# Performance work log

Measured on AMD Instinct MI355X. Metric: run time of the kernel, lower is better.

The kernel has to match this reference:

```python
import jax, jax.numpy as jnp
import numpy as np

NUM_HEADS = 8
EPS = 1e-5


def setup_inputs() -> dict:
    key = jax.random.key(0)
    ks = jax.random.split(key, 7)
    B, C, H, W, D = 1, 256, 16, 16, 16
    return {
        "x": jax.random.normal(ks[0], (B, C, H, W, D), dtype=jnp.float32),
        "w_dw": jax.random.normal(ks[1], (C, 1, 3, 3, 3), dtype=jnp.float32) * 0.05,
        "b_dw": jax.random.normal(ks[2], (C,), dtype=jnp.float32) * 0.05,
        "w_qkv": jax.random.normal(ks[3], (3 * C, C), dtype=jnp.float32) * 0.05,
        "b_qkv": jax.random.normal(ks[4], (3 * C,), dtype=jnp.float32) * 0.05,
        "w_proj": jax.random.normal(ks[5], (C, C), dtype=jnp.float32) * 0.05,
        "b_proj": jax.random.normal(ks[6], (C,), dtype=jnp.float32) * 0.05,
    }


def reference(x, w_dw, b_dw, w_qkv, b_qkv, w_proj, b_proj):
    B, C, H, W, D = x.shape
    nh = NUM_HEADS
    hd = C // nh
    scale = hd ** (-0.5)
    N = H * W * D

    # depthwise 3x3x3 conv (groups=C), SAME padding
    y = jax.lax.conv_general_dilated(
        x, w_dw, window_strides=(1, 1, 1), padding="SAME",
        dimension_numbers=("NCHWD", "OIHWD", "NCHWD"),
        feature_group_count=C,
    ) + b_dw[None, :, None, None, None]

    # InstanceNorm3d (affine=False): normalize over spatial dims per (b, c)
    mu = y.mean(axis=(2, 3, 4), keepdims=True)
    var = y.var(axis=(2, 3, 4), keepdims=True)
    y = (y - mu) * jax.lax.rsqrt(var + EPS)

    # 1x1x1 conv -> 3*C channels
    qkv = jnp.einsum("bchwd,oc->bohwd", y, w_qkv) + b_qkv[None, :, None, None, None]

    # [B, 3, nh, hd, N] -> q, k, v each [B, nh, N, hd]
    qkv = qkv.reshape(B, 3, nh, hd, N)
    q, k, v = jnp.transpose(qkv, (1, 0, 2, 4, 3))

    attn = jax.nn.softmax(jnp.einsum("bhnd,bhmd->bhnm", q, k) * scale, axis=-1)
    out = jnp.einsum("bhnm,bhmd->bhnd", attn, v)  # [B, nh, N, hd]

    # transpose(-1, -2) then reshape to [B, C, H, W, D]
    out = jnp.transpose(out, (0, 1, 3, 2)).reshape(B, C, H, W, D)

    # output 1x1x1 projection
    out = jnp.einsum("bchwd,oc->bohwd", out, w_proj) + b_proj[None, :, None, None, None]
    return out
```

## Files before the change

kernel.cpp:

```cpp
#include <hip/hip_runtime.h>
#include <hip/hip_bf16.h>

#define NSP 4096
#define QSC2 0.25503486f

typedef __attribute__((ext_vector_type(8))) short bf16x8;
typedef __attribute__((ext_vector_type(4))) float f32x4;
typedef __attribute__((ext_vector_type(16))) float f32x16;

__device__ __forceinline__ unsigned short f2bf(float f){
  union{float f;unsigned int u;}c; c.f=f;
  unsigned int r = c.u + 0x7fffu + ((c.u>>16)&1u);
  return (unsigned short)(r>>16);
}
__device__ __forceinline__ unsigned int pk2(float a, float b){
  __hip_bfloat162 p = __float22bfloat162_rn(make_float2(a, b));
  unsigned int r; __builtin_memcpy(&r, &p, 4); return r;
}
__device__ __forceinline__ ushort4 pk4(float a, float b, float c, float d){
  union { ushort4 u4; uint2 u2; } u;
  u.u2.x = pk2(a, b); u.u2.y = pk2(c, d);
  return u.u4;
}

__global__ __launch_bounds__(512) void k_dwconv(
    const float* __restrict__ x,
    const float* __restrict__ wdw,
    const float* __restrict__ bdw,
    unsigned short* __restrict__ ybn)
{
  const int c = blockIdx.x;
  const int tid = threadIdx.x;
  __shared__ float xs[4096];
  __shared__ float wsh[27];
  __shared__ float bsh;
  __shared__ float rs[8], rq[8];

  const float* xc = x + (size_t)c * NSP;
  for (int i = tid; i < 1024; i += 512) *(float4*)&xs[i*4] = ((const float4*)xc)[i];
  if (tid < 27) wsh[tid] = wdw[c*27 + tid];
  if (tid == 31) bsh = bdw[c];
  __syncthreads();

  float yv[8];
  float sum = 0.f, sumsq = 0.f;
  #pragma unroll
  for (int i = 0; i < 8; i++){
    const int n = (i << 9) + tid;
    const int h = n >> 8, w = (n >> 4) & 15, d = n & 15;
    float acc = bsh;
    #pragma unroll
    for (int kh = 0; kh < 3; kh++){
      const int hh = h + kh - 1;
      if ((unsigned)hh >= 16u) continue;
      #pragma unroll
      for (int kw = 0; kw < 3; kw++){
        const int ww = w + kw - 1;
        if ((unsigned)ww >= 16u) continue;
        #pragma unroll
        for (int kd = 0; kd < 3; kd++){
          const int dd = d + kd - 1;
          if ((unsigned)dd >= 16u) continue;
          acc += wsh[kh*9 + kw*3 + kd] * xs[(hh<<8) + (ww<<4) + dd];
        }
      }
    }
    yv[i] = acc; sum += acc; sumsq += acc*acc;
  }
  #pragma unroll
  for (int off = 32; off > 0; off >>= 1){
    sum   += __shfl_down(sum, off, 64);
    sumsq += __shfl_down(sumsq, off, 64);
  }
  const int wid = tid >> 6, lane = tid & 63;
  if (lane == 0){ rs[wid] = sum; rq[wid] = sumsq; }
  __syncthreads();
  float ts = 0.f, tq = 0.f;
  #pragma unroll
  for (int i = 0; i < 8; i++){ ts += rs[i]; tq += rq[i]; }
  const float mean = ts * (1.f/4096.f);
  const float var  = tq * (1.f/4096.f) - mean*mean;
  const float rinv = rsqrtf(var + 1e-5f);
  unsigned short* yo = ybn + (size_t)c * NSP;
  #pragma unroll
  for (int i = 0; i < 8; i++) yo[(i<<9) + tid] = f2bf((yv[i] - mean) * rinv);
}

__global__ __launch_bounds__(256) void k_trans(
    const unsigned short* __restrict__ ybn,
    unsigned short* __restrict__ ynT)
{
  __shared__ unsigned short T[64][72];
  const int tid = threadIdx.x;
  const int n0 = blockIdx.x * 64, c0 = blockIdx.y * 64;
  const int cl = tid >> 4, n4 = (tid & 15) * 4;
  #pragma unroll
  for (int i = 0; i < 4; i++){
    const int c = cl + i*16;
    const ushort4 v = *(const ushort4*)(ybn + (size_t)(c0 + c) * NSP + n0 + n4);
    T[n4+0][c] = v.x; T[n4+1][c] = v.y; T[n4+2][c] = v.z; T[n4+3][c] = v.w;
  }
  __syncthreads();
  const int nl = tid >> 2, s8 = (tid & 3) * 16;
  *(uint4*)(ynT + (size_t)(n0+nl)*256 + c0 + s8)     = *(const uint4*)&T[nl][s8];
  *(uint4*)(ynT + (size_t)(n0+nl)*256 + c0 + s8 + 8) = *(const uint4*)&T[nl][s8 + 8];
}

__global__ __launch_bounds__(256) void k_qkv(
    const float* __restrict__ wqkv,
    const float* __restrict__ bqkv,
    const unsigned short* __restrict__ ynT,
    unsigned short* __restrict__ qb, unsigned short* __restrict__ kb,
    unsigned short* __restrict__ vbt)
{
  __shared__ unsigned short Wb[64][264];
  const int tid = threadIdx.x;
  const int o0 = blockIdx.y * 64;
  const int n0 = blockIdx.x * 128;
  {
    const int row = tid & 63, part = tid >> 6;
    const float* src = wqkv + (size_t)(o0 + row) * 256 + part * 64;
    unsigned short* dst = &Wb[row][part*64];
    #pragma unroll
    for (int j = 0; j < 8; j++){
      const float4 a = ((const float4*)src)[2*j];
      const float4 b = ((const float4*)src)[2*j+1];
      *(ushort4*)&dst[j*8]     = pk4(a.x, a.y, a.z, a.w);
      *(ushort4*)&dst[j*8 + 4] = pk4(b.x, b.y, b.z, b.w);
    }
  }
  __syncthreads();

  const int w = tid >> 6, lane = tid & 63, quad = lane >> 4, cc = lane & 15;
  const int nbase = n0 + w*32;
  const bool isv = (o0 >= 512);
  f32x4 acc[2][4] = {};

  #pragma unroll
  for (int k = 0; k < 8; k++){
    const bf16x8 y0 = *(const bf16x8*)(ynT + (size_t)(nbase + cc)  * 256 + k*32 + quad*8);
    const bf16x8 y1 = *(const bf16x8*)(ynT + (size_t)(nbase+16+cc) * 256 + k*32 + quad*8);
    #pragma unroll
    for (int os = 0; os < 4; os++){
      const bf16x8 wf = *(const bf16x8*)&Wb[os*16 + cc][k*32 + quad*8];
      if (!isv){
        acc[0][os] = __builtin_amdgcn_mfma_f32_16x16x32_bf16(y0, wf, acc[0][os], 0, 0, 0);
        acc[1][os] = __builtin_amdgcn_mfma_f32_16x16x32_bf16(y1, wf, acc[1][os], 0, 0, 0);
      } else {
        acc[0][os] = __builtin_amdgcn_mfma_f32_16x16x32_bf16(wf, y0, acc[0][os], 0, 0, 0);
        acc[1][os] = __builtin_amdgcn_mfma_f32_16x16x32_bf16(wf, y1, acc[1][os], 0, 0, 0);
      }
    }
  }

  if (!isv){
    #pragma unroll
    for (int os = 0; os < 4; os++){
      const int o = o0 + os*16 + cc;
      const int g = o >> 8, hh = (o >> 5) & 7, dd = o & 31;
      const float bias = bqkv[o];
      const float sc = (g == 0) ? QSC2 : 1.f;
      unsigned short* dst = (g == 0) ? qb : kb;
      #pragma unroll
      for (int ns = 0; ns < 2; ns++){
        #pragma unroll
        for (int r = 0; r < 4; r++){
          const int n = nbase + ns*16 + quad*4 + r;
          dst[((size_t)hh * NSP + n) * 32 + dd] = f2bf((acc[ns][os][r] + bias) * sc);
        }
      }
    }
  } else {
    #pragma unroll
    for (int os = 0; os < 4; os++){
      #pragma unroll
      for (int r = 0; r < 4; r++){
        const int orow = o0 - 512 + os*16 + quad*4 + r;
        const float bias = bqkv[512 + orow];
        #pragma unroll
        for (int ns = 0; ns < 2; ns++){
          const int n = nbase + ns*16 + cc;
          vbt[(size_t)orow * NSP + n] = f2bf(acc[ns][os][r] + bias);
        }
      }
    }
  }
}

__global__ __launch_bounds__(128) void k_attn(
    const unsigned short* __restrict__ qb,
    const unsigned short* __restrict__ kb,
    const unsigned short* __restrict__ vbt,
    float* __restrict__ op, float* __restrict__ lp, int ktlen)
{
  const int h = blockIdx.y, q0 = blockIdx.x * 64, z = blockIdx.z;
  const int tid = threadIdx.x;
  const int w = tid >> 6, l = tid & 63;
  const int lq = l & 31, lb = l >> 5;

  __shared__ unsigned short ks [64][40];
  __shared__ unsigned short vsT[32][72];
  __shared__ unsigned short pst[64][72];

  const int qg = q0 + w*32 + lq;
  const bf16x8 qf0 = *(const bf16x8*)(qb + ((size_t)(h*NSP + qg))*32 + lb*8);
  const bf16x8 qf1 = *(const bf16x8*)(qb + ((size_t)(h*NSP + qg))*32 + 16 + lb*8);
  const unsigned short* kbase = kb  + (size_t)h * NSP * 32;
  const unsigned short* vbase = vbt + (size_t)h * 32 * NSP;

  f32x16 oacc = {};
  float lsum = 0.f;

  const int kt0 = z * ktlen;
  const int krow = tid >> 1, kseg = (tid & 1) * 16;
  const int vrow = tid >> 2, vseg = (tid & 3) * 16;
  const int iters = ktlen >> 6;

  for (int it = 0; it < iters; it++){
    const int kt = kt0 + it * 64;
    {
      const uint4* src = (const uint4*)(kbase + (size_t)(kt + krow) * 32 + kseg);
      const uint4 a = src[0], b = src[1];
      *(uint4*)&ks[krow][kseg]     = a;
      *(uint4*)&ks[krow][kseg + 8] = b;
      const uint4* vs = (const uint4*)(vbase + (size_t)vrow * NSP + kt + vseg);
      const uint4 c = vs[0], d = vs[1];
      *(uint4*)&vsT[vrow][vseg]     = c;
      *(uint4*)&vsT[vrow][vseg + 8] = d;
    }
    __syncthreads();

    #pragma unroll
    for (int t2 = 0; t2 < 2; t2++){
      const bf16x8 af0 = *(const bf16x8*)&ks[t2*32 + lq][lb*8];
      const bf16x8 af1 = *(const bf16x8*)&ks[t2*32 + lq][16 + lb*8];
      f32x16 sa = {};
      sa = __builtin_amdgcn_mfma_f32_32x32x16_bf16(af0, qf0, sa, 0, 0, 0);
      sa = __builtin_amdgcn_mfma_f32_32x32x16_bf16(af1, qf1, sa, 0, 0, 0);
      #pragma unroll
      for (int g = 0; g < 4; g++){
        const float p0 = exp2f(sa[g*4+0]), p1 = exp2f(sa[g*4+1]);
        const float p2 = exp2f(sa[g*4+2]), p3 = exp2f(sa[g*4+3]);
        lsum += (p0 + p1) + (p2 + p3);
        *(ushort4*)&pst[w*32 + lq][t2*32 + g*8 + lb*4] = pk4(p0, p1, p2, p3);
      }
    }
    #pragma unroll
    for (int ck = 0; ck < 4; ck++){
      const bf16x8 vf = *(const bf16x8*)&vsT[lq]       [ck*16 + lb*8];
      const bf16x8 pf = *(const bf16x8*)&pst[w*32 + lq][ck*16 + lb*8];
      oacc = __builtin_amdgcn_mfma_f32_32x32x16_bf16(vf, pf, oacc, 0, 0, 0);
    }
    __syncthreads();
  }

  lsum += __shfl_xor(lsum, 32, 64);

  float* dst = op + ((size_t)z * NSP + qg) * 256 + h*32;
  #pragma unroll
  for (int g = 0; g < 4; g++){
    f32x4 v = { oacc[g*4+0], oacc[g*4+1], oacc[g*4+2], oacc[g*4+3] };
    *(f32x4*)(dst + g*8 + lb*4) = v;
  }
  if (lb == 0) lp[((size_t)z * 8 + h) * NSP + qg] = lsum;
}

__global__ __launch_bounds__(256) void k_proj(
    const float* __restrict__ wproj,
    const float* __restrict__ bproj,
    const float* __restrict__ op,
    const float* __restrict__ lp,
    float* __restrict__ out, int nz)
{
  __shared__ unsigned short Wb[64][264];
  const int tid = threadIdx.x;
  const int o0 = blockIdx.y * 64;
  const int n0 = blockIdx.x * 128;
  {
    const int row = tid & 63, part = tid >> 6;
    const float* src = wproj + (size_t)(o0 + row) * 256 + part * 64;
    unsigned short* dst = &Wb[row][part*64];
    #pragma unroll
    for (int j = 0; j < 8; j++){
      const float4 a = ((const float4*)src)[2*j];
      const float4 b = ((const float4*)src)[2*j+1];
      *(ushort4*)&dst[j*8]     = pk4(a.x, a.y, a.z, a.w);
      *(ushort4*)&dst[j*8 + 4] = pk4(b.x, b.y, b.z, b.w);
    }
  }
  __syncthreads();

  const int w = tid >> 6, lane = tid & 63, quad = lane >> 4, cc = lane & 15;
  const int nbase = n0 + w*32;
  f32x4 acc[2][4] = {};

  #pragma unroll
  for (int k = 0; k < 8; k++){
    const int n0r = nbase + cc, n1r = nbase + 16 + cc;
    float l0 = 0.f, l1 = 0.f;
    f32x4 s00 = {}, s01 = {}, s10 = {}, s11 = {};
    for (int z = 0; z < nz; z++){
      l0 += lp[((size_t)z*8 + k) * NSP + n0r];
      l1 += lp[((size_t)z*8 + k) * NSP + n1r];
      const float* p0 = op + ((size_t)z * NSP + n0r) * 256 + k*32 + quad*8;
      const float* p1 = op + ((size_t)z * NSP + n1r) * 256 + k*32 + quad*8;
      s00 += *(const f32x4*)p0;  s01 += *(const f32x4*)(p0 + 4);
      s10 += *(const f32x4*)p1;  s11 += *(const f32x4*)(p1 + 4);
    }
    const float r0 = 1.f / l0, r1 = 1.f / l1;
    union { bf16x8 v; ushort4 u[2]; } y0u, y1u;
    y0u.u[0] = pk4(s00[0]*r0, s00[1]*r0, s00[2]*r0, s00[3]*r0);
    y0u.u[1] = pk4(s01[0]*r0, s01[1]*r0, s01[2]*r0, s01[3]*r0);
    y1u.u[0] = pk4(s10[0]*r1, s10[1]*r1, s10[2]*r1, s10[3]*r1);
    y1u.u[1] = pk4(s11[0]*r1, s11[1]*r1, s11[2]*r1, s11[3]*r1);
    #pragma unroll
    for (int os = 0; os < 4; os++){
      const bf16x8 wf = *(const bf16x8*)&Wb[os*16 + cc][k*32 + quad*8];
      acc[0][os] = __builtin_amdgcn_mfma_f32_16x16x32_bf16(wf, y0u.v, acc[0][os], 0, 0, 0);
      acc[1][os] = __builtin_amdgcn_mfma_f32_16x16x32_bf16(wf, y1u.v, acc[1][os], 0, 0, 0);
    }
  }

  #pragma unroll
  for (int os = 0; os < 4; os++){
    #pragma unroll
    for (int r = 0; r < 4; r++){
      const int o = o0 + os*16 + quad*4 + r;
      const float bias = bproj[o];
      #pragma unroll
      for (int ns = 0; ns < 2; ns++){
        const int n = nbase + ns*16 + cc;
        out[(size_t)o * NSP + n] = acc[ns][os][r] + bias;
      }
    }
  }
}

extern "C" void kernel_launch(void* const* d_in, const int* in_sizes, int n_in,
                              void* d_out, int out_size, void* d_ws, size_t ws_size,
                              hipStream_t stream) {
  (void)in_sizes; (void)n_in; (void)out_size;
  const float* x     = (const float*)d_in[0];
  const float* wdw   = (const float*)d_in[1];
  const float* bdw   = (const float*)d_in[2];
  const float* wqkv  = (const float*)d_in[3];
  const float* bqkv  = (const float*)d_in[4];
  const float* wproj = (const float*)d_in[5];
  const float* bproj = (const float*)d_in[6];
  float* out = (float*)d_out;

  const int nz = (ws_size >= ((size_t)24 << 20)) ? 4 : 2;
  const int ktlen = NSP / nz;

  char* ws = (char*)d_ws;
  const size_t opB = (size_t)nz << 22;
  float*          op  = (float*)ws;
  unsigned short* ybn = (unsigned short*)ws;
  unsigned short* ynT = (unsigned short*)(ws + (2<<20));
  unsigned short* qb  = (unsigned short*)(ws + opB);
  unsigned short* kb  = (unsigned short*)(ws + opB + (2<<20));
  unsigned short* vbt = (unsigned short*)(ws + opB + (4<<20));
  float*          lp  = (float*)(ws + opB + (6<<20));

  k_dwconv <<<dim3(256),        dim3(512), 0, stream>>>(x, wdw, bdw, ybn);
  k_trans  <<<dim3(64, 4),      dim3(256), 0, stream>>>(ybn, ynT);
  k_qkv    <<<dim3(32, 12),     dim3(256), 0, stream>>>(wqkv, bqkv, ynT, qb, kb, vbt);
  k_attn   <<<dim3(64, 8, nz),  dim3(128), 0, stream>>>(qb, kb, vbt, op, lp, ktlen);
  k_proj   <<<dim3(32, 4),      dim3(256), 0, stream>>>(wproj, bproj, op, lp, out, nz);
}
```

Measured before the change: 168.1 us.

## Store split-K attention partials in bf16 and halve qkv/proj tile size

```diff
diff --git a/kernel.cpp b/kernel.cpp
--- a/kernel.cpp
+++ b/kernel.cpp
@@ -21,6 +21,9 @@
   union { ushort4 u4; uint2 u2; } u;
   u.u2.x = pk2(a, b); u.u2.y = pk2(c, d);
   return u.u4;
+}
+__device__ __forceinline__ float bfu2f(unsigned short u){
+  union { unsigned int i; float f; } c; c.i = ((unsigned int)u) << 16; return c.f;
 }
 
 __global__ __launch_bounds__(512) void k_dwconv(
@@ -116,7 +119,7 @@
   __shared__ unsigned short Wb[64][264];
   const int tid = threadIdx.x;
   const int o0 = blockIdx.y * 64;
-  const int n0 = blockIdx.x * 128;
+  const int n0 = blockIdx.x * 64;
   {
     const int row = tid & 63, part = tid >> 6;
     const float* src = wqkv + (size_t)(o0 + row) * 256 + part * 64;
@@ -132,24 +135,18 @@
   __syncthreads();
 
   const int w = tid >> 6, lane = tid & 63, quad = lane >> 4, cc = lane & 15;
-  const int nbase = n0 + w*32;
+  const int nbase = n0 + w*16;
   const bool isv = (o0 >= 512);
-  f32x4 acc[2][4] = {};
+  f32x4 acc[4] = {};
 
   #pragma unroll
   for (int k = 0; k < 8; k++){
-    const bf16x8 y0 = *(const bf16x8*)(ynT + (size_t)(nbase + cc)  * 256 + k*32 + quad*8);
-    const bf16x8 y1 = *(const bf16x8*)(ynT + (size_t)(nbase+16+cc) * 256 + k*32 + quad*8);
+    const bf16x8 y0 = *(const bf16x8*)(ynT + (size_t)(nbase + cc) * 256 + k*32 + quad*8);
     #pragma unroll
     for (int os = 0; os < 4; os++){
       const bf16x8 wf = *(const bf16x8*)&Wb[os*16 + cc][k*32 + quad*8];
-      if (!isv){
-        acc[0][os] = __builtin_amdgcn_mfma_f32_16x16x32_bf16(y0, wf, acc[0][os], 0, 0, 0);
-        acc[1][os] = __builtin_amdgcn_mfma_f32_16x16x32_bf16(y1, wf, acc[1][os], 0, 0, 0);
-      } else {
-        acc[0][os] = __builtin_amdgcn_mfma_f32_16x16x32_bf16(wf, y0, acc[0][os], 0, 0, 0);
-        acc[1][os] = __builtin_amdgcn_mfma_f32_16x16x32_bf16(wf, y1, acc[1][os], 0, 0, 0);
-      }
+      if (!isv) acc[os] = __builtin_amdgcn_mfma_f32_16x16x32_bf16(y0, wf, acc[os], 0, 0, 0);
+      else      acc[os] = __builtin_amdgcn_mfma_f32_16x16x32_bf16(wf, y0, acc[os], 0, 0, 0);
     }
   }
 
@@ -162,12 +159,9 @@
       const float sc = (g == 0) ? QSC2 : 1.f;
       unsigned short* dst = (g == 0) ? qb : kb;
       #pragma unroll
-      for (int ns = 0; ns < 2; ns++){
-        #pragma unroll
-        for (int r = 0; r < 4; r++){
-          const int n = nbase + ns*16 + quad*4 + r;
-          dst[((size_t)hh * NSP + n) * 32 + dd] = f2bf((acc[ns][os][r] + bias) * sc);
-        }
+      for (int r = 0; r < 4; r++){
+        const int n = nbase + quad*4 + r;
+        dst[((size_t)hh * NSP + n) * 32 + dd] = f2bf((acc[os][r] + bias) * sc);
       }
     }
   } else {
@@ -177,11 +171,8 @@
       for (int r = 0; r < 4; r++){
         const int orow = o0 - 512 + os*16 + quad*4 + r;
         const float bias = bqkv[512 + orow];
-        #pragma unroll
-        for (int ns = 0; ns < 2; ns++){
-          const int n = nbase + ns*16 + cc;
-          vbt[(size_t)orow * NSP + n] = f2bf(acc[ns][os][r] + bias);
-        }
+        const int n = nbase + cc;
+        vbt[(size_t)orow * NSP + n] = f2bf(acc[os][r] + bias);
       }
     }
   }
@@ -191,7 +182,7 @@
     const unsigned short* __restrict__ qb,
     const unsigned short* __restrict__ kb,
     const unsigned short* __restrict__ vbt,
-    float* __restrict__ op, float* __restrict__ lp, int ktlen)
+    unsigned short* __restrict__ opb, float* __restrict__ lp, int ktlen)
 {
   const int h = blockIdx.y, q0 = blockIdx.x * 64, z = blockIdx.z;
   const int tid = threadIdx.x;
@@ -256,11 +247,11 @@
 
   lsum += __shfl_xor(lsum, 32, 64);
 
-  float* dst = op + ((size_t)z * NSP + qg) * 256 + h*32;
+  unsigned short* dst = opb + ((size_t)z * NSP + qg) * 256 + h*32;
   #pragma unroll
   for (int g = 0; g < 4; g++){
-    f32x4 v = { oacc[g*4+0], oacc[g*4+1], oacc[g*4+2], oacc[g*4+3] };
-    *(f32x4*)(dst + g*8 + lb*4) = v;
+    *(ushort4*)(dst + g*8 + lb*4) =
+        pk4(oacc[g*4+0], oacc[g*4+1], oacc[g*4+2], oacc[g*4+3]);
   }
   if (lb == 0) lp[((size_t)z * 8 + h) * NSP + qg] = lsum;
 }
@@ -268,14 +259,14 @@
 __global__ __launch_bounds__(256) void k_proj(
     const float* __restrict__ wproj,
     const float* __restrict__ bproj,
-    const float* __restrict__ op,
+    const unsigned short* __restrict__ opb,
     const float* __restrict__ lp,
     float* __restrict__ out, int nz)
 {
   __shared__ unsigned short Wb[64][264];
   const int tid = threadIdx.x;
   const int o0 = blockIdx.y * 64;
-  const int n0 = blockIdx.x * 128;
+  const int n0 = blockIdx.x * 64;
   {
     const int row = tid & 63, part = tid >> 6;
     const float* src = wproj + (size_t)(o0 + row) * 256 + part * 64;
@@ -291,33 +282,28 @@
   __syncthreads();
 
   const int w = tid >> 6, lane = tid & 63, quad = lane >> 4, cc = lane & 15;
-  const int nbase = n0 + w*32;
-  f32x4 acc[2][4] = {};
+  const int nr = n0 + w*16 + cc;
+  f32x4 acc[4] = {};
 
   #pragma unroll
   for (int k = 0; k < 8; k++){
-    const int n0r = nbase + cc, n1r = nbase + 16 + cc;
-    float l0 = 0.f, l1 = 0.f;
-    f32x4 s00 = {}, s01 = {}, s10 = {}, s11 = {};
+    float lt = 0.f;
+    float s[8] = {};
     for (int z = 0; z < nz; z++){
-      l0 += lp[((size_t)z*8 + k) * NSP + n0r];
-      l1 += lp[((size_t)z*8 + k) * NSP + n1r];
-      const float* p0 = op + ((size_t)z * NSP + n0r) * 256 + k*32 + quad*8;
-      const float* p1 = op + ((size_t)z * NSP + n1r) * 256 + k*32 + quad*8;
-      s00 += *(const f32x4*)p0;  s01 += *(const f32x4*)(p0 + 4);
-      s10 += *(const f32x4*)p1;  s11 += *(const f32x4*)(p1 + 4);
-    }
-    const float r0 = 1.f / l0, r1 = 1.f / l1;
-    union { bf16x8 v; ushort4 u[2]; } y0u, y1u;
-    y0u.u[0] = pk4(s00[0]*r0, s00[1]*r0, s00[2]*r0, s00[3]*r0);
-    y0u.u[1] = pk4(s01[0]*r0, s01[1]*r0, s01[2]*r0, s01[3]*r0);
-    y1u.u[0] = pk4(s10[0]*r1, s10[1]*r1, s10[2]*r1, s10[3]*r1);
-    y1u.u[1] = pk4(s11[0]*r1, s11[1]*r1, s11[2]*r1, s11[3]*r1);
+      lt += lp[((size_t)z*8 + k) * NSP + nr];
+      union { uint4 q; unsigned short u[8]; } v;
+      v.q = *(const uint4*)(opb + ((size_t)z * NSP + nr) * 256 + k*32 + quad*8);
+      #pragma unroll
+      for (int j = 0; j < 8; j++) s[j] += bfu2f(v.u[j]);
+    }
+    const float r = 1.f / lt;
+    union { bf16x8 v; ushort4 u[2]; } yb;
+    yb.u[0] = pk4(s[0]*r, s[1]*r, s[2]*r, s[3]*r);
+    yb.u[1] = pk4(s[4]*r, s[5]*r, s[6]*r, s[7]*r);
     #pragma unroll
     for (int os = 0; os < 4; os++){
       const bf16x8 wf = *(const bf16x8*)&Wb[os*16 + cc][k*32 + quad*8];
-      acc[0][os] = __builtin_amdgcn_mfma_f32_16x16x32_bf16(wf, y0u.v, acc[0][os], 0, 0, 0);
-      acc[1][os] = __builtin_amdgcn_mfma_f32_16x16x32_bf16(wf, y1u.v, acc[1][os], 0, 0, 0);
+      acc[os] = __builtin_amdgcn_mfma_f32_16x16x32_bf16(wf, yb.v, acc[os], 0, 0, 0);
     }
   }
 
@@ -326,12 +312,7 @@
     #pragma unroll
     for (int r = 0; r < 4; r++){
       const int o = o0 + os*16 + quad*4 + r;
-      const float bias = bproj[o];
-      #pragma unroll
-      for (int ns = 0; ns < 2; ns++){
-        const int n = nbase + ns*16 + cc;
-        out[(size_t)o * NSP + n] = acc[ns][os][r] + bias;
-      }
+      out[(size_t)o * NSP + nr] = acc[os][r] + bproj[o];
     }
   }
 }
@@ -349,12 +330,12 @@
   const float* bproj = (const float*)d_in[6];
   float* out = (float*)d_out;
 
-  const int nz = (ws_size >= ((size_t)24 << 20)) ? 4 : 2;
+  const int nz = (ws_size >= ((size_t)16 << 20)) ? 4 : 2;
   const int ktlen = NSP / nz;
 
   char* ws = (char*)d_ws;
-  const size_t opB = (size_t)nz << 22;
-  float*          op  = (float*)ws;
+  const size_t opB = (size_t)nz << 21;
+  unsigned short* opb = (unsigned short*)ws;
   unsigned short* ybn = (unsigned short*)ws;
   unsigned short* ynT = (unsigned short*)(ws + (2<<20));
   unsigned short* qb  = (unsigned short*)(ws + opB);
@@ -364,7 +345,7 @@
 
   k_dwconv <<<dim3(256),        dim3(512), 0, stream>>>(x, wdw, bdw, ybn);
   k_trans  <<<dim3(64, 4),      dim3(256), 0, stream>>>(ybn, ynT);
-  k_qkv    <<<dim3(32, 12),     dim3(256), 0, stream>>>(wqkv, bqkv, ynT, qb, kb, vbt);
-  k_attn   <<<dim3(64, 8, nz),  dim3(128), 0, stream>>>(qb, kb, vbt, op, lp, ktlen);
-  k_proj   <<<dim3(32, 4),      dim3(256), 0, stream>>>(wproj, bproj, op, lp, out, nz);
-}
+  k_qkv    <<<dim3(64, 12),     dim3(256), 0, stream>>>(wqkv, bqkv, ynT, qb, kb, vbt);
+  k_attn   <<<dim3(64, 8, nz),  dim3(128), 0, stream>>>(qb, kb, vbt, opb, lp, ktlen);
+  k_proj   <<<dim3(64, 4),      dim3(256), 0, stream>>>(wproj, bproj, opb, lp, out, nz);
+}
```

Result: faster. 160.3 us (-4.6%).
